# Kernel optimization log

Measured on AMD Instinct MI355X. Metric: run time of the kernel, lower is better.

The kernel has to match this reference:

```python
import jax, jax.numpy as jnp
import numpy as np

B, T, D, N = 16, 4096, 512, 3


def _window_sum(x, k):
    # x: [B, T, ...] -> sliding-window sum of size k, stride 1 -> [B, T-k+1, ...]
    c = jnp.cumsum(x, axis=1)
    c = jnp.concatenate([jnp.zeros_like(c[:, :1]), c], axis=1)
    return c[:, k:] - c[:, :-k]


def setup_inputs() -> dict:
    key = jax.random.key(0)
    ks = jax.random.split(key, 7)
    s_prev = jax.random.normal(ks[0], (B, D), jnp.float32)
    enc_hs = jax.random.normal(ks[1], (B, T, D), jnp.float32)
    # realistic padding mask: True = padded position
    lengths = jax.random.randint(ks[2], (B,), T // 2, T + 1)
    src_mask = jnp.arange(T)[None, :] >= lengths[:, None]
    scale = 1.0 / np.sqrt(D)
    Vw = jax.random.normal(ks[3], (N, D, D), jnp.float32) * scale
    Vb = jax.random.normal(ks[4], (N, D), jnp.float32) * 0.01
    Ww = jax.random.normal(ks[5], (N, D, D), jnp.float32) * scale
    Wb = jax.random.normal(ks[6], (N, D), jnp.float32) * 0.01
    return {"s_prev": s_prev, "enc_hs": enc_hs, "src_mask": src_mask,
            "Vw": Vw, "Vb": Vb, "Ww": Ww, "Wb": Wb}


def _level(s_prev, hs, mask, vw, vb, ww, wb):
    # hs: [B, L, D], mask: [B, L] (True = masked)
    # torch Linear: y = x @ W^T + b, weight is [out, in]
    v = jnp.einsum('bld,ed->ble', hs, vw) + vb            # V_i(hs)
    att = jnp.einsum('bd,bld->bl', s_prev, v)             # bmm(s_prev, V(hs)^T)
    att = jnp.where(mask, -jnp.inf, att)
    att = jax.nn.softmax(att, axis=-1)                    # [B, L]
    pooled = jnp.einsum('bl,bld->bd', att, hs)            # bmm(att, hs)
    ctx = pooled @ ww.T + wb                              # W_i(.)
    return ctx, att


def reference(s_prev, enc_hs, src_mask, Vw, Vb, Ww, Wb):
    ctx, att = _level(s_prev, enc_hs, src_mask, Vw[0], Vb[0], Ww[0], Wb[0])
    for i in range(1, N):
        k = i + 1
        hs_ngram = _window_sum(enc_hs, k) / k                      # AvgPool1d(k,1)
        n_mask = _window_sum(src_mask.astype(jnp.float32), k) > 0  # any masked in window
        c, _ = _level(s_prev, hs_ngram, n_mask, Vw[i], Vb[i], Ww[i], Wb[i])
        ctx = ctx + c
    return ctx, att
```

## Files before the change

### kernel.cpp

```cpp
#include <hip/hip_runtime.h>

#define BB 16
#define TT 4096
#define DD 512
#define CH 32
#define NY (TT/CH)
#define NEG (-1.0e30f)

#define OFF_Q     64
#define OFF_QP    (OFF_Q + 3*BB*DD)
#define OFF_P0    (OFF_QP + 4*3*BB*DD)
#define OFF_M     (OFF_P0 + BB*TT)
#define OFF_S     (OFF_M + 3*BB*NY)
#define OFF_SC    (OFF_S + 3*BB*NY)
#define OFF_PART  (OFF_SC + 3*BB*NY)
#define OFF_POOL  (OFF_PART + 3*NY*BB*DD)

__global__ void __launch_bounds__(256) k_lengths(const unsigned char* mask, int* lengths) {
    __shared__ int sflag;
    __shared__ int sred[4];
    const int tid = threadIdx.x;
    const int b = blockIdx.x;
    if (tid == 0) sflag = 0;
    __syncthreads();
    int f = 0;
    for (int idx = tid * 4 + 1; idx < BB * TT; idx += 256 * 4)
        f |= (mask[idx] != 0);
    if (f) atomicOr(&sflag, 1);
    __syncthreads();
    const bool byte_layout = (sflag != 0);
    const int* m32 = (const int*)mask;
    int cnt = 0;
    if (byte_layout) {
        for (int t = tid; t < TT; t += 256) cnt += (mask[b * TT + t] != 0);
    } else {
        for (int t = tid; t < TT; t += 256) cnt += (m32[b * TT + t] != 0);
    }
    #pragma unroll
    for (int m = 32; m >= 1; m >>= 1) cnt += __shfl_xor(cnt, m, 64);
    if ((tid & 63) == 0) sred[tid >> 6] = cnt;
    __syncthreads();
    if (tid == 0)
        lengths[b] = TT - (sred[0] + sred[1] + sred[2] + sred[3]);
}

__global__ void __launch_bounds__(256) k_q(const float* __restrict__ s_prev,
                                           const float* __restrict__ Vw,
                                           float* __restrict__ qpart) {
    const int blk = blockIdx.x;
    const int ec = blk & 3;
    const int ib = blk >> 2;
    const int b = ib % BB;
    const int i = ib / BB;
    const int d0 = threadIdx.x;
    const float* sp = s_prev + b * DD + ec * 128;
    const float* W = Vw + (size_t)i * DD * DD + (size_t)(ec * 128) * DD;
    float a0 = 0.f, a1 = 0.f;
    for (int e = 0; e < 128; e++) {
        const float se = sp[e];
        a0 += se * W[e * DD + d0];
        a1 += se * W[e * DD + d0 + 256];
    }
    qpart[(size_t)blk * DD + d0] = a0;
    qpart[(size_t)blk * DD + d0 + 256] = a1;
}

__global__ void __launch_bounds__(256) k_q_reduce(const float* __restrict__ qpart,
                                                  float* __restrict__ q) {
    const int idx = blockIdx.x * 256 + threadIdx.x;
    const int ib = idx / DD;
    const int d = idx % DD;
    float s = 0.f;
    #pragma unroll
    for (int ec = 0; ec < 4; ec++) s += qpart[(size_t)(ib * 4 + ec) * DD + d];
    q[idx] = s;
}

__global__ void __launch_bounds__(256) k_fused(const float* __restrict__ enc,
                                               const float* __restrict__ q,
                                               const int* __restrict__ lengths,
                                               float* __restrict__ p0,
                                               float* __restrict__ mbuf,
                                               float* __restrict__ sbuf,
                                               float* __restrict__ part) {
    __shared__ float sp[CH + 2][3];
    __shared__ float svs[3][CH];
    __shared__ float su[3][CH];
    __shared__ float sm[3];
    const int b = blockIdx.x;
    const int y = blockIdx.y;
    const int t0 = y * CH;
    const int len = lengths[b];
    const int tid = threadIdx.x;
    if (t0 >= len) {
        if (tid < 3) {
            mbuf[(size_t)(tid * BB + b) * NY + y] = NEG;
            sbuf[(size_t)(tid * BB + b) * NY + y] = 0.f;
        }
        return;
    }
    const int wv = tid >> 6, lane = tid & 63;

    const float4* q40 = (const float4*)(q + (size_t)(0 * BB + b) * DD);
    const float4* q41 = (const float4*)(q + (size_t)(1 * BB + b) * DD);
    const float4* q42 = (const float4*)(q + (size_t)(2 * BB + b) * DD);
    const float4 qa0 = q40[lane], qb0 = q40[64 + lane];
    const float4 qa1 = q41[lane], qb1 = q41[64 + lane];
    const float4 qa2 = q42[lane], qb2 = q42[64 + lane];
    #pragma unroll
    for (int rr = 0; rr < CH / 4 + 1; rr++) {
        if (rr == CH / 4 && wv >= 2) break;
        const int r = (rr < CH / 4) ? (wv + rr * 4) : (CH + wv);
        const int t = t0 + r;
        float d0 = 0.f, d1 = 0.f, d2 = 0.f;
        if (t < len) {
            const float4* e4 = (const float4*)(enc + ((size_t)b * TT + t) * DD);
            const float4 x0 = e4[lane], x1 = e4[64 + lane];
            d0 = x0.x*qa0.x + x0.y*qa0.y + x0.z*qa0.z + x0.w*qa0.w
               + x1.x*qb0.x + x1.y*qb0.y + x1.z*qb0.z + x1.w*qb0.w;
            d1 = x0.x*qa1.x + x0.y*qa1.y + x0.z*qa1.z + x0.w*qa1.w
               + x1.x*qb1.x + x1.y*qb1.y + x1.z*qb1.z + x1.w*qb1.w;
            d2 = x0.x*qa2.x + x0.y*qa2.y + x0.z*qa2.z + x0.w*qa2.w
               + x1.x*qb2.x + x1.y*qb2.y + x1.z*qb2.z + x1.w*qb2.w;
            #pragma unroll
            for (int m = 32; m >= 1; m >>= 1) {
                d0 += __shfl_xor(d0, m, 64);
                d1 += __shfl_xor(d1, m, 64);
                d2 += __shfl_xor(d2, m, 64);
            }
        }
        if (lane == 0) {
            sp[r][0] = d0; sp[r][1] = d1; sp[r][2] = d2;
            if (rr < CH / 4 && t < len) p0[(size_t)b * TT + t] = d0;
        }
    }
    __syncthreads();

    if (tid < 3 * CH) {
        const int i = tid / CH, r = tid % CH;
        const int l = t0 + r;
        const bool valid = l < (len - i);
        float s = sp[r][i];
        if (i > 0) s += sp[r + 1][i];
        if (i > 1) s += sp[r + 2][i];
        svs[i][r] = valid ? s * (1.0f / (float)(i + 1)) : NEG;
    }
    __syncthreads();
    if (tid < 3) {
        float m = NEG;
        #pragma unroll
        for (int r = 0; r < CH; r++) m = fmaxf(m, svs[tid][r]);
        sm[tid] = m;
    }
    __syncthreads();
    if (tid < 3 * CH) {
        const int i = tid / CH, r = tid % CH;
        const bool valid = (t0 + r) < (len - i);
        su[i][r] = valid ? __expf(svs[i][r] - sm[i]) : 0.f;
    }
    __syncthreads();
    if (tid < 3) {
        float s = 0.f;
        #pragma unroll
        for (int r = 0; r < CH; r++) s += su[tid][r];
        mbuf[(size_t)(tid * BB + b) * NY + y] = sm[tid];
        sbuf[(size_t)(tid * BB + b) * NY + y] = s;
    }
    __syncthreads();

    const int d = tid * 2;
    const float* col = enc + (size_t)b * TT * DD + d;
    float2 va, vb2, vc;
    {
        const int t = t0;
        va  = (t     < TT) ? *(const float2*)(col + (size_t)t * DD)       : make_float2(0.f, 0.f);
        vb2 = (t + 1 < TT) ? *(const float2*)(col + (size_t)(t + 1) * DD) : make_float2(0.f, 0.f);
    }
    float2 a0 = {0, 0}, a1 = {0, 0}, a2 = {0, 0};
    #pragma unroll
    for (int r = 0; r < CH; r++) {
        const int t = t0 + r;
        vc = (t + 2 < TT) ? *(const float2*)(col + (size_t)(t + 2) * DD) : make_float2(0.f, 0.f);
        const float u0 = su[0][r], u1 = su[1][r], u2 = su[2][r];
        const float w1x = va.x + vb2.x, w1y = va.y + vb2.y;
        const float w2x = w1x + vc.x,   w2y = w1y + vc.y;
        a0.x += u0 * va.x;  a0.y += u0 * va.y;
        a1.x += u1 * w1x;   a1.y += u1 * w1y;
        a2.x += u2 * w2x;   a2.y += u2 * w2y;
        va = vb2; vb2 = vc;
    }
    a1.x *= 0.5f; a1.y *= 0.5f;
    a2.x *= (1.0f / 3.0f); a2.y *= (1.0f / 3.0f);
    float* pt = part + (size_t)y * BB * DD + (size_t)b * DD + d;
    *(float2*)(pt)                            = a0;
    *(float2*)(pt + (size_t)NY * BB * DD)     = a1;
    *(float2*)(pt + (size_t)2 * NY * BB * DD) = a2;
}

__global__ void __launch_bounds__(256) k_combine(const float* __restrict__ mbuf,
                                                 const float* __restrict__ sbuf,
                                                 const float* __restrict__ p0,
                                                 const int* __restrict__ lengths,
                                                 float* __restrict__ scale,
                                                 float* __restrict__ att) {
    __shared__ float sred[4];
    __shared__ float sbc;
    const int g = blockIdx.x;
    const int i = g / BB, b = g % BB;
    const int tid = threadIdx.x;
    const float ml = (tid < NY) ? mbuf[(size_t)g * NY + tid] : NEG;
    const float sl = (tid < NY) ? sbuf[(size_t)g * NY + tid] : 0.f;
    float v = ml;
    #pragma unroll
    for (int m = 32; m >= 1; m >>= 1) v = fmaxf(v, __shfl_xor(v, m, 64));
    if ((tid & 63) == 0) sred[tid >> 6] = v;
    __syncthreads();
    if (tid == 0) sbc = fmaxf(fmaxf(sred[0], sred[1]), fmaxf(sred[2], sred[3]));
    __syncthreads();
    const float gm = sbc;
    __syncthreads();
    const float e = (tid < NY) ? __expf(ml - gm) : 0.f;
    v = sl * e;
    #pragma unroll
    for (int m = 32; m >= 1; m >>= 1) v += __shfl_xor(v, m, 64);
    if ((tid & 63) == 0) sred[tid >> 6] = v;
    __syncthreads();
    if (tid == 0) sbc = sred[0] + sred[1] + sred[2] + sred[3];
    __syncthreads();
    const float inv = 1.0f / sbc;
    if (tid < NY) scale[(size_t)g * NY + tid] = e * inv;
    if (i == 0) {
        const int len = lengths[b];
        for (int t = tid; t < TT; t += 256)
            att[(size_t)b * TT + t] =
                (t < len) ? __expf(p0[(size_t)b * TT + t] - gm) * inv : 0.f;
    }
}

__global__ void __launch_bounds__(256) k_reduce(const float* __restrict__ part,
                                                const float* __restrict__ scale,
                                                float* __restrict__ pooled) {
    const int idx = blockIdx.x * 256 + threadIdx.x;
    const int ib = idx / DD;
    const int d = idx % DD;
    const int i = ib / BB, b = ib % BB;
    const float* sc = scale + (size_t)ib * NY;
    const float* base = part + (size_t)i * NY * BB * DD + (size_t)b * DD + d;
    float s = 0.f;
    #pragma unroll 8
    for (int y = 0; y < NY; y++) s += base[(size_t)y * BB * DD] * sc[y];
    pooled[idx] = s;
}

__global__ void __launch_bounds__(256) k_ctx(const float* __restrict__ pooled,
                                             const float* __restrict__ Ww,
                                             const float* __restrict__ Wb,
                                             float* __restrict__ ctx) {
    const int wid = blockIdx.x * 4 + (threadIdx.x >> 6);
    const int lane = threadIdx.x & 63;
    const int b = wid >> 9;
    const int e = wid & 511;
    float acc = 0.f;
    #pragma unroll
    for (int i = 0; i < 3; i++) {
        const float4* pr = (const float4*)(pooled + (size_t)(i * BB + b) * DD);
        const float4* wr = (const float4*)(Ww + ((size_t)i * DD + e) * DD);
        const float4 p0 = pr[lane], p1 = pr[64 + lane];
        const float4 w0 = wr[lane], w1 = wr[64 + lane];
        acc += p0.x * w0.x + p0.y * w0.y + p0.z * w0.z + p0.w * w0.w
             + p1.x * w1.x + p1.y * w1.y + p1.z * w1.z + p1.w * w1.w;
    }
    #pragma unroll
    for (int m = 32; m >= 1; m >>= 1) acc += __shfl_xor(acc, m, 64);
    if (lane == 0)
        ctx[(size_t)b * DD + e] = acc + Wb[e] + Wb[DD + e] + Wb[2 * DD + e];
}

extern "C" void kernel_launch(void* const* d_in, const int* in_sizes, int n_in,
                              void* d_out, int out_size, void* d_ws, size_t ws_size,
                              hipStream_t stream) {
    const float* s_prev = (const float*)d_in[0];
    const float* enc    = (const float*)d_in[1];
    const void*  mask   = d_in[2];
    const float* Vw     = (const float*)d_in[3];
    const float* Ww     = (const float*)d_in[5];
    const float* Wb     = (const float*)d_in[6];

    float* out = (float*)d_out;
    float* ctx = out;
    float* att = out + BB * DD;

    float* W       = (float*)d_ws;
    int*   lengths = (int*)d_ws;
    float* q       = W + OFF_Q;
    float* qpart   = W + OFF_QP;
    float* p0      = W + OFF_P0;
    float* mbuf    = W + OFF_M;
    float* sbuf    = W + OFF_S;
    float* scale   = W + OFF_SC;
    float* part    = W + OFF_PART;
    float* pooled  = W + OFF_POOL;

    k_lengths<<<BB, 256, 0, stream>>>((const unsigned char*)mask, lengths);
    k_q<<<192, 256, 0, stream>>>(s_prev, Vw, qpart);
    k_q_reduce<<<3 * BB * DD / 256, 256, 0, stream>>>(qpart, q);
    k_fused<<<dim3(BB, NY), 256, 0, stream>>>(enc, q, lengths, p0, mbuf, sbuf, part);
    k_combine<<<3 * BB, 256, 0, stream>>>(mbuf, sbuf, p0, lengths, scale, att);
    k_reduce<<<3 * BB * DD / 256, 256, 0, stream>>>(part, scale, pooled);
    k_ctx<<<BB * DD / 4, 256, 0, stream>>>(pooled, Ww, Wb, ctx);
}
```

Measured before the change: 275.5 us.

## Halve chunk size and use half-wave groups per row in scores kernel

Reduces the time-chunk per block from 32 to 16 rows, doubling the number of blocks, and reassigns each encoder row's dot products to a 32-lane group instead of a full 64-lane wave. Each lane now accumulates four float4 loads before a shorter 5-step shuffle reduction. This aims to raise parallelism and cut shuffle overhead, but doubles the partial-sum buffer written and read in the reduce stage. The combine kernel drops its bounds guards because NY now equals the block size of 256.

```diff
diff --git a/kernel.cpp b/kernel.cpp
--- a/kernel.cpp
+++ b/kernel.cpp
@@ -3,7 +3,7 @@
 #define BB 16
 #define TT 4096
 #define DD 512
-#define CH 32
+#define CH 16
 #define NY (TT/CH)
 #define NEG (-1.0e30f)
 
@@ -99,39 +99,45 @@
         }
         return;
     }
-    const int wv = tid >> 6, lane = tid & 63;
+    const int grp = tid >> 5;
+    const int sl = tid & 31;
 
     const float4* q40 = (const float4*)(q + (size_t)(0 * BB + b) * DD);
     const float4* q41 = (const float4*)(q + (size_t)(1 * BB + b) * DD);
     const float4* q42 = (const float4*)(q + (size_t)(2 * BB + b) * DD);
-    const float4 qa0 = q40[lane], qb0 = q40[64 + lane];
-    const float4 qa1 = q41[lane], qb1 = q41[64 + lane];
-    const float4 qa2 = q42[lane], qb2 = q42[64 + lane];
-    #pragma unroll
-    for (int rr = 0; rr < CH / 4 + 1; rr++) {
-        if (rr == CH / 4 && wv >= 2) break;
-        const int r = (rr < CH / 4) ? (wv + rr * 4) : (CH + wv);
+    float4 qf0[4], qf1[4], qf2[4];
+    #pragma unroll
+    for (int j = 0; j < 4; j++) {
+        qf0[j] = q40[sl + 32 * j];
+        qf1[j] = q41[sl + 32 * j];
+        qf2[j] = q42[sl + 32 * j];
+    }
+
+    #pragma unroll
+    for (int rr = 0; rr < 3; rr++) {
+        if (rr == 2 && grp >= 2) break;
+        const int r = (rr < 2) ? (grp + 8 * rr) : (CH + grp);
         const int t = t0 + r;
         float d0 = 0.f, d1 = 0.f, d2 = 0.f;
         if (t < len) {
             const float4* e4 = (const float4*)(enc + ((size_t)b * TT + t) * DD);
-            const float4 x0 = e4[lane], x1 = e4[64 + lane];
-            d0 = x0.x*qa0.x + x0.y*qa0.y + x0.z*qa0.z + x0.w*qa0.w
-               + x1.x*qb0.x + x1.y*qb0.y + x1.z*qb0.z + x1.w*qb0.w;
-            d1 = x0.x*qa1.x + x0.y*qa1.y + x0.z*qa1.z + x0.w*qa1.w
-               + x1.x*qb1.x + x1.y*qb1.y + x1.z*qb1.z + x1.w*qb1.w;
-            d2 = x0.x*qa2.x + x0.y*qa2.y + x0.z*qa2.z + x0.w*qa2.w
-               + x1.x*qb2.x + x1.y*qb2.y + x1.z*qb2.z + x1.w*qb2.w;
             #pragma unroll
-            for (int m = 32; m >= 1; m >>= 1) {
-                d0 += __shfl_xor(d0, m, 64);
-                d1 += __shfl_xor(d1, m, 64);
-                d2 += __shfl_xor(d2, m, 64);
+            for (int j = 0; j < 4; j++) {
+                const float4 x = e4[sl + 32 * j];
+                d0 += x.x * qf0[j].x + x.y * qf0[j].y + x.z * qf0[j].z + x.w * qf0[j].w;
+                d1 += x.x * qf1[j].x + x.y * qf1[j].y + x.z * qf1[j].z + x.w * qf1[j].w;
+                d2 += x.x * qf2[j].x + x.y * qf2[j].y + x.z * qf2[j].z + x.w * qf2[j].w;
             }
         }
-        if (lane == 0) {
+        #pragma unroll
+        for (int m = 16; m >= 1; m >>= 1) {
+            d0 += __shfl_xor(d0, m, 32);
+            d1 += __shfl_xor(d1, m, 32);
+            d2 += __shfl_xor(d2, m, 32);
+        }
+        if (sl == 0) {
             sp[r][0] = d0; sp[r][1] = d1; sp[r][2] = d2;
-            if (rr < CH / 4 && t < len) p0[(size_t)b * TT + t] = d0;
+            if (r < CH && t < len) p0[(size_t)b * TT + t] = d0;
         }
     }
     __syncthreads();
@@ -208,8 +214,8 @@
     const int g = blockIdx.x;
     const int i = g / BB, b = g % BB;
     const int tid = threadIdx.x;
-    const float ml = (tid < NY) ? mbuf[(size_t)g * NY + tid] : NEG;
-    const float sl = (tid < NY) ? sbuf[(size_t)g * NY + tid] : 0.f;
+    const float ml = mbuf[(size_t)g * NY + tid];
+    const float sl = sbuf[(size_t)g * NY + tid];
     float v = ml;
     #pragma unroll
     for (int m = 32; m >= 1; m >>= 1) v = fmaxf(v, __shfl_xor(v, m, 64));
@@ -219,7 +225,7 @@
     __syncthreads();
     const float gm = sbc;
     __syncthreads();
-    const float e = (tid < NY) ? __expf(ml - gm) : 0.f;
+    const float e = __expf(ml - gm);
     v = sl * e;
     #pragma unroll
     for (int m = 32; m >= 1; m >>= 1) v += __shfl_xor(v, m, 64);
@@ -228,7 +234,7 @@
     if (tid == 0) sbc = sred[0] + sred[1] + sred[2] + sred[3];
     __syncthreads();
     const float inv = 1.0f / sbc;
-    if (tid < NY) scale[(size_t)g * NY + tid] = e * inv;
+    scale[(size_t)g * NY + tid] = e * inv;
     if (i == 0) {
         const int len = lengths[b];
         for (int t = tid; t < TT; t += 256)
```

After: 271.1 us. No clear change (-1.6%).
